# Optimization experiments

Measured on AMD Instinct MI355X. Metric: run time of the kernel, lower is better.

## Reference

```python
import jax, jax.numpy as jnp
import numpy as np

N = 50000
E = 800000
DIMS = [(8, 16), (16, 16), (16, 16)]  # (in, out) per layer


def setup_inputs() -> dict:
    key = jax.random.key(0)
    ks = jax.random.split(key, 32)
    inp = {}
    inp['x'] = jax.random.normal(ks[0], (N, 8), dtype=jnp.float32)
    inp['pos'] = jax.random.normal(ks[1], (N, 3), dtype=jnp.float32)
    k = 2
    for i, (ci, co) in enumerate(DIMS):
        d = ci * co
        inp[f'lin_w{i}'] = jax.random.normal(ks[k], (3, d), dtype=jnp.float32); k += 1
        inp[f'lin_b{i}'] = jax.random.normal(ks[k], (d,), dtype=jnp.float32); k += 1
        inp[f'gamma{i}'] = jax.random.normal(ks[k], (d,), dtype=jnp.float32); k += 1
        inp[f'beta{i}'] = jax.random.normal(ks[k], (d,), dtype=jnp.float32); k += 1
        inp[f'root{i}'] = jax.random.normal(ks[k], (ci, co), dtype=jnp.float32); k += 1
        inp[f'bias{i}'] = jax.random.normal(ks[k], (co,), dtype=jnp.float32); k += 1
    inp['batch'] = jnp.zeros((N,), dtype=jnp.int32)
    inp['idx'] = jnp.sort(jax.random.randint(ks[k], (25000,), 0, N, dtype=jnp.int32)); k += 1
    inp['edge_index'] = jax.random.randint(ks[k], (2, E), 0, N, dtype=jnp.int32)
    return inp


def _nnconv(x, pseudo, src, dst, lin_w, lin_b, gamma, beta, root, bias, ci, co):
    # edge MLP (Linear -> batchnorm(eval, affine) -> ReLU), plain_last=False
    w = jax.nn.relu((pseudo @ lin_w + lin_b) * gamma + beta)  # [E, ci*co]
    w = w.reshape(-1, ci, co)                                  # [E, ci, co]
    msg = jnp.einsum('ei,eio->eo', x[src], w)                  # per-edge vec-mat
    s = jax.ops.segment_sum(msg, dst, num_segments=N)          # scatter-sum
    cnt = jax.ops.segment_sum(jnp.ones((msg.shape[0],), x.dtype), dst, num_segments=N)
    aggr = s / jnp.maximum(cnt, 1.0)[:, None]                  # scatter-mean
    return aggr + x @ root + bias


def reference(x, pos, lin_w0, lin_b0, gamma0, beta0, root0, bias0,
              lin_w1, lin_b1, gamma1, beta1, root1, bias1,
              lin_w2, lin_b2, gamma2, beta2, root2, bias2,
              batch, idx, edge_index):
    src, dst = edge_index[0], edge_index[1]
    pseudo = pos[dst] - pos[src]  # patch_size is None
    params = [
        (lin_w0, lin_b0, gamma0, beta0, root0, bias0),
        (lin_w1, lin_b1, gamma1, beta1, root1, bias1),
        (lin_w2, lin_b2, gamma2, beta2, root2, bias2),
    ]
    h = x
    for (ci, co), p in zip(DIMS, params):
        h = jax.nn.relu(_nnconv(h, pseudo, src, dst, *p, ci, co))  # drop_act=False
    return h[idx], pos[idx], batch[idx]
```

## Files before the change

kernel.cpp:

```cpp
#include <hip/hip_runtime.h>

#define N_NODES 50000
#define N_EDGES 800000
#define M_IDX   25000
#define DMAX    64

__global__ __launch_bounds__(256) void prep_kernel(
    const int*   __restrict__ ei,
    const float* __restrict__ pos,
    float4*      __restrict__ pseudo,
    int*         __restrict__ cnt,
    int*         __restrict__ adj,
    int E)
{
    int e = blockIdx.x * blockDim.x + threadIdx.x;
    if (e >= E) return;
    int s = ei[e];
    int t = ei[E + e];
    float4 pd;
    pd.x = pos[t * 3 + 0] - pos[s * 3 + 0];
    pd.y = pos[t * 3 + 1] - pos[s * 3 + 1];
    pd.z = pos[t * 3 + 2] - pos[s * 3 + 2];
    pd.w = __int_as_float(s);
    pseudo[e] = pd;
    int p = atomicAdd(&cnt[t], 1);
    if (p < DMAX) adj[t * DMAX + p] = e;
}

template<int CI>
__global__ __launch_bounds__(256) void edge_msg_kernel(
    const float4* __restrict__ pseudo,
    const float*  __restrict__ h_in,
    const float*  __restrict__ lin_w,
    const float*  __restrict__ lin_b,
    const float*  __restrict__ gamma,
    const float*  __restrict__ beta,
    float*        __restrict__ mbuf,
    int E)
{
    const int o = threadIdx.x & 15;
    const int d = CI * 16;
    float W0[CI], W1[CI], W2[CI], B[CI];
#pragma unroll
    for (int i = 0; i < CI; ++i) {
        int j = i * 16 + o;
        float g = gamma[j];
        W0[i] = lin_w[j] * g;
        W1[i] = lin_w[d + j] * g;
        W2[i] = lin_w[2 * d + j] * g;
        B[i]  = fmaf(lin_b[j], g, beta[j]);
    }
    const int g   = (blockIdx.x * blockDim.x + threadIdx.x) >> 4;
    const int ng  = (gridDim.x * blockDim.x) >> 4;

    for (int e0 = g; e0 < E; e0 += 2 * ng) {
        const int e1 = e0 + ng;
        const bool v1 = (e1 < E);
        float4 pd0 = pseudo[e0];
        float4 pd1 = v1 ? pseudo[e1] : pd0;
        const int s0 = __float_as_int(pd0.w);
        const int s1 = __float_as_int(pd1.w);
        float x0[CI], x1[CI];
        const float4* xp0 = (const float4*)(h_in + (size_t)s0 * CI);
        const float4* xp1 = (const float4*)(h_in + (size_t)s1 * CI);
#pragma unroll
        for (int q = 0; q < CI / 4; ++q) {
            float4 a = xp0[q];
            x0[4 * q + 0] = a.x; x0[4 * q + 1] = a.y;
            x0[4 * q + 2] = a.z; x0[4 * q + 3] = a.w;
            float4 b = xp1[q];
            x1[4 * q + 0] = b.x; x1[4 * q + 1] = b.y;
            x1[4 * q + 2] = b.z; x1[4 * q + 3] = b.w;
        }
        float a0 = 0.f, a1 = 0.f;
#pragma unroll
        for (int i = 0; i < CI; ++i) {
            float w0 = fmaf(pd0.z, W2[i], fmaf(pd0.y, W1[i], fmaf(pd0.x, W0[i], B[i])));
            a0 = fmaf(x0[i], fmaxf(w0, 0.f), a0);
            float w1 = fmaf(pd1.z, W2[i], fmaf(pd1.y, W1[i], fmaf(pd1.x, W0[i], B[i])));
            a1 = fmaf(x1[i], fmaxf(w1, 0.f), a1);
        }
        mbuf[(size_t)e0 * 16 + o] = a0;
        if (v1) mbuf[(size_t)e1 * 16 + o] = a1;
    }
}

template<int CI>
__global__ __launch_bounds__(256) void node_reduce_kernel(
    const int*   __restrict__ adj,
    const int*   __restrict__ cnt,
    const float* __restrict__ mbuf,
    const float* __restrict__ h_in,
    const float* __restrict__ root,
    const float* __restrict__ bias,
    float*       __restrict__ h_out,
    int N)
{
    int tid = blockIdx.x * blockDim.x + threadIdx.x;
    if (tid >= N * 16) return;
    const int t = tid >> 4, o = tid & 15;
    const int deg = cnt[t];
    const int dl  = min(deg, DMAX);
    const int4* arow = (const int4*)(adj + (size_t)t * DMAX);
    float acc = 0.f;
    const int rounds = (dl + 3) >> 2;
    for (int r = 0; r < rounds; ++r) {
        int4 e4 = arow[r];
        int base = r * 4;
        bool m0 = base + 0 < dl, m1 = base + 1 < dl;
        bool m2 = base + 2 < dl, m3 = base + 3 < dl;
        int i0 = m0 ? e4.x : 0, i1 = m1 ? e4.y : 0;
        int i2 = m2 ? e4.z : 0, i3 = m3 ? e4.w : 0;
        float v0 = mbuf[(size_t)i0 * 16 + o];
        float v1 = mbuf[(size_t)i1 * 16 + o];
        float v2 = mbuf[(size_t)i2 * 16 + o];
        float v3 = mbuf[(size_t)i3 * 16 + o];
        acc += (m0 ? v0 : 0.f) + (m1 ? v1 : 0.f) + (m2 ? v2 : 0.f) + (m3 ? v3 : 0.f);
    }
    float r = fmaf(acc, 1.0f / fmaxf((float)deg, 1.0f), bias[o]);
    const float4* hp = (const float4*)(h_in + (size_t)t * CI);
#pragma unroll
    for (int q = 0; q < CI / 4; ++q) {
        float4 v = hp[q];
        r = fmaf(v.x, root[(4 * q + 0) * 16 + o], r);
        r = fmaf(v.y, root[(4 * q + 1) * 16 + o], r);
        r = fmaf(v.z, root[(4 * q + 2) * 16 + o], r);
        r = fmaf(v.w, root[(4 * q + 3) * 16 + o], r);
    }
    h_out[tid] = fmaxf(r, 0.f);
}

__global__ __launch_bounds__(256) void gather_kernel(
    const float* __restrict__ h,
    const float* __restrict__ pos,
    const int*   __restrict__ batch,
    const int*   __restrict__ idx,
    float*       __restrict__ out,
    int M)
{
    int j = blockIdx.x * blockDim.x + threadIdx.x;
    if (j >= M) return;
    int n = idx[j];
    float4*       o4 = (float4*)out + (size_t)j * 4;
    const float4* h4 = (const float4*)(h + (size_t)n * 16);
    o4[0] = h4[0]; o4[1] = h4[1]; o4[2] = h4[2]; o4[3] = h4[3];
    float* po = out + (size_t)M * 16 + (size_t)j * 3;
    po[0] = pos[n * 3 + 0];
    po[1] = pos[n * 3 + 1];
    po[2] = pos[n * 3 + 2];
    ((int*)out)[(size_t)M * 19 + j] = batch[n];
}

extern "C" void kernel_launch(void* const* d_in, const int* in_sizes, int n_in,
                              void* d_out, int out_size, void* d_ws, size_t ws_size,
                              hipStream_t stream) {
    const float* x      = (const float*)d_in[0];
    const float* pos    = (const float*)d_in[1];
    const float* lin_w0 = (const float*)d_in[2];
    const float* lin_b0 = (const float*)d_in[3];
    const float* gamma0 = (const float*)d_in[4];
    const float* beta0  = (const float*)d_in[5];
    const float* root0  = (const float*)d_in[6];
    const float* bias0  = (const float*)d_in[7];
    const float* lin_w1 = (const float*)d_in[8];
    const float* lin_b1 = (const float*)d_in[9];
    const float* gamma1 = (const float*)d_in[10];
    const float* beta1  = (const float*)d_in[11];
    const float* root1  = (const float*)d_in[12];
    const float* bias1  = (const float*)d_in[13];
    const float* lin_w2 = (const float*)d_in[14];
    const float* lin_b2 = (const float*)d_in[15];
    const float* gamma2 = (const float*)d_in[16];
    const float* beta2  = (const float*)d_in[17];
    const float* root2  = (const float*)d_in[18];
    const float* bias2  = (const float*)d_in[19];
    const int*   batch  = (const int*)d_in[20];
    const int*   idx    = (const int*)d_in[21];
    const int*   ei     = (const int*)d_in[22];
    float*       out    = (float*)d_out;

    float4* pseudo = (float4*)d_ws;
    float*  mbuf   = (float*)(pseudo + N_EDGES);
    int*    adj    = (int*)(mbuf + (size_t)N_EDGES * 16);
    float*  hA     = (float*)(adj + (size_t)N_NODES * DMAX);
    float*  hB     = hA + (size_t)N_NODES * 16;
    int*    cnt    = (int*)(hB + (size_t)N_NODES * 16);

    const int EB = 2048;
    const int NB = (N_NODES * 16 + 255) / 256;

    hipMemsetAsync(cnt, 0, N_NODES * sizeof(int), stream);
    prep_kernel<<<(N_EDGES + 255) / 256, 256, 0, stream>>>(ei, pos, pseudo, cnt, adj, N_EDGES);

    edge_msg_kernel<8><<<EB, 256, 0, stream>>>(pseudo, x, lin_w0, lin_b0, gamma0, beta0, mbuf, N_EDGES);
    node_reduce_kernel<8><<<NB, 256, 0, stream>>>(adj, cnt, mbuf, x, root0, bias0, hA, N_NODES);

    edge_msg_kernel<16><<<EB, 256, 0, stream>>>(pseudo, hA, lin_w1, lin_b1, gamma1, beta1, mbuf, N_EDGES);
    node_reduce_kernel<16><<<NB, 256, 0, stream>>>(adj, cnt, mbuf, hA, root1, bias1, hB, N_NODES);

    edge_msg_kernel<16><<<EB, 256, 0, stream>>>(pseudo, hB, lin_w2, lin_b2, gamma2, beta2, mbuf, N_EDGES);
    node_reduce_kernel<16><<<NB, 256, 0, stream>>>(adj, cnt, mbuf, hB, root2, bias2, hA, N_NODES);

    gather_kernel<<<(M_IDX + 255) / 256, 256, 0, stream>>>(hA, pos, batch, idx, out, M_IDX);
}
```

Before: 325.8 us.

## Fuse edge message computation into per-node reduction with destination-sorted edge data

```diff
diff --git a/kernel.cpp b/kernel.cpp
--- a/kernel.cpp
+++ b/kernel.cpp
@@ -8,38 +8,42 @@
 __global__ __launch_bounds__(256) void prep_kernel(
     const int*   __restrict__ ei,
     const float* __restrict__ pos,
-    float4*      __restrict__ pseudo,
     int*         __restrict__ cnt,
-    int*         __restrict__ adj,
+    float4*      __restrict__ pdata,
     int E)
 {
     int e = blockIdx.x * blockDim.x + threadIdx.x;
     if (e >= E) return;
+    int t = ei[E + e];
     int s = ei[e];
-    int t = ei[E + e];
+    int p = atomicAdd(&cnt[t], 1);
     float4 pd;
     pd.x = pos[t * 3 + 0] - pos[s * 3 + 0];
     pd.y = pos[t * 3 + 1] - pos[s * 3 + 1];
     pd.z = pos[t * 3 + 2] - pos[s * 3 + 2];
     pd.w = __int_as_float(s);
-    pseudo[e] = pd;
-    int p = atomicAdd(&cnt[t], 1);
-    if (p < DMAX) adj[t * DMAX + p] = e;
+    if (p < DMAX) pdata[(size_t)t * DMAX + p] = pd;
 }
 
 template<int CI>
-__global__ __launch_bounds__(256) void edge_msg_kernel(
-    const float4* __restrict__ pseudo,
+__global__ __launch_bounds__(256) void node_fused_kernel(
+    const float4* __restrict__ pdata,
+    const int*    __restrict__ cnt,
     const float*  __restrict__ h_in,
     const float*  __restrict__ lin_w,
     const float*  __restrict__ lin_b,
     const float*  __restrict__ gamma,
     const float*  __restrict__ beta,
-    float*        __restrict__ mbuf,
-    int E)
+    const float*  __restrict__ root,
+    const float*  __restrict__ bias,
+    float*        __restrict__ h_out,
+    int N)
 {
-    const int o = threadIdx.x & 15;
+    int tid = blockIdx.x * blockDim.x + threadIdx.x;
+    if (tid >= N * 16) return;
+    const int t = tid >> 4, o = tid & 15;
     const int d = CI * 16;
+
     float W0[CI], W1[CI], W2[CI], B[CI];
 #pragma unroll
     for (int i = 0; i < CI; ++i) {
@@ -50,19 +54,19 @@
         W2[i] = lin_w[2 * d + j] * g;
         B[i]  = fmaf(lin_b[j], g, beta[j]);
     }
-    const int g   = (blockIdx.x * blockDim.x + threadIdx.x) >> 4;
-    const int ng  = (gridDim.x * blockDim.x) >> 4;
 
-    for (int e0 = g; e0 < E; e0 += 2 * ng) {
-        const int e1 = e0 + ng;
-        const bool v1 = (e1 < E);
-        float4 pd0 = pseudo[e0];
-        float4 pd1 = v1 ? pseudo[e1] : pd0;
-        const int s0 = __float_as_int(pd0.w);
-        const int s1 = __float_as_int(pd1.w);
+    const int deg = cnt[t];
+    const int dl  = min(deg, DMAX);
+    const float4* __restrict__ row = pdata + (size_t)t * DMAX;
+
+    float acc = 0.f;
+    int p = 0;
+    for (; p + 2 <= dl; p += 2) {
+        float4 pd0 = row[p];
+        float4 pd1 = row[p + 1];
+        const float4* xp0 = (const float4*)(h_in + (size_t)__float_as_int(pd0.w) * CI);
+        const float4* xp1 = (const float4*)(h_in + (size_t)__float_as_int(pd1.w) * CI);
         float x0[CI], x1[CI];
-        const float4* xp0 = (const float4*)(h_in + (size_t)s0 * CI);
-        const float4* xp1 = (const float4*)(h_in + (size_t)s1 * CI);
 #pragma unroll
         for (int q = 0; q < CI / 4; ++q) {
             float4 a = xp0[q];
@@ -72,51 +76,31 @@
             x1[4 * q + 0] = b.x; x1[4 * q + 1] = b.y;
             x1[4 * q + 2] = b.z; x1[4 * q + 3] = b.w;
         }
-        float a0 = 0.f, a1 = 0.f;
 #pragma unroll
         for (int i = 0; i < CI; ++i) {
             float w0 = fmaf(pd0.z, W2[i], fmaf(pd0.y, W1[i], fmaf(pd0.x, W0[i], B[i])));
-            a0 = fmaf(x0[i], fmaxf(w0, 0.f), a0);
+            acc = fmaf(x0[i], fmaxf(w0, 0.f), acc);
             float w1 = fmaf(pd1.z, W2[i], fmaf(pd1.y, W1[i], fmaf(pd1.x, W0[i], B[i])));
-            a1 = fmaf(x1[i], fmaxf(w1, 0.f), a1);
+            acc = fmaf(x1[i], fmaxf(w1, 0.f), acc);
         }
-        mbuf[(size_t)e0 * 16 + o] = a0;
-        if (v1) mbuf[(size_t)e1 * 16 + o] = a1;
     }
-}
+    if (p < dl) {
+        float4 pd0 = row[p];
+        const float4* xp0 = (const float4*)(h_in + (size_t)__float_as_int(pd0.w) * CI);
+        float x0[CI];
+#pragma unroll
+        for (int q = 0; q < CI / 4; ++q) {
+            float4 a = xp0[q];
+            x0[4 * q + 0] = a.x; x0[4 * q + 1] = a.y;
+            x0[4 * q + 2] = a.z; x0[4 * q + 3] = a.w;
+        }
+#pragma unroll
+        for (int i = 0; i < CI; ++i) {
+            float w0 = fmaf(pd0.z, W2[i], fmaf(pd0.y, W1[i], fmaf(pd0.x, W0[i], B[i])));
+            acc = fmaf(x0[i], fmaxf(w0, 0.f), acc);
+        }
+    }
 
-template<int CI>
-__global__ __launch_bounds__(256) void node_reduce_kernel(
-    const int*   __restrict__ adj,
-    const int*   __restrict__ cnt,
-    const float* __restrict__ mbuf,
-    const float* __restrict__ h_in,
-    const float* __restrict__ root,
-    const float* __restrict__ bias,
-    float*       __restrict__ h_out,
-    int N)
-{
-    int tid = blockIdx.x * blockDim.x + threadIdx.x;
-    if (tid >= N * 16) return;
-    const int t = tid >> 4, o = tid & 15;
-    const int deg = cnt[t];
-    const int dl  = min(deg, DMAX);
-    const int4* arow = (const int4*)(adj + (size_t)t * DMAX);
-    float acc = 0.f;
-    const int rounds = (dl + 3) >> 2;
-    for (int r = 0; r < rounds; ++r) {
-        int4 e4 = arow[r];
-        int base = r * 4;
-        bool m0 = base + 0 < dl, m1 = base + 1 < dl;
-        bool m2 = base + 2 < dl, m3 = base + 3 < dl;
-        int i0 = m0 ? e4.x : 0, i1 = m1 ? e4.y : 0;
-        int i2 = m2 ? e4.z : 0, i3 = m3 ? e4.w : 0;
-        float v0 = mbuf[(size_t)i0 * 16 + o];
-        float v1 = mbuf[(size_t)i1 * 16 + o];
-        float v2 = mbuf[(size_t)i2 * 16 + o];
-        float v3 = mbuf[(size_t)i3 * 16 + o];
-        acc += (m0 ? v0 : 0.f) + (m1 ? v1 : 0.f) + (m2 ? v2 : 0.f) + (m3 ? v3 : 0.f);
-    }
     float r = fmaf(acc, 1.0f / fmaxf((float)deg, 1.0f), bias[o]);
     const float4* hp = (const float4*)(h_in + (size_t)t * CI);
 #pragma unroll
@@ -179,27 +163,22 @@
     const int*   ei     = (const int*)d_in[22];
     float*       out    = (float*)d_out;
 
-    float4* pseudo = (float4*)d_ws;
-    float*  mbuf   = (float*)(pseudo + N_EDGES);
-    int*    adj    = (int*)(mbuf + (size_t)N_EDGES * 16);
-    float*  hA     = (float*)(adj + (size_t)N_NODES * DMAX);
-    float*  hB     = hA + (size_t)N_NODES * 16;
-    int*    cnt    = (int*)(hB + (size_t)N_NODES * 16);
+    float4* pdata = (float4*)d_ws;
+    float*  hA    = (float*)(pdata + (size_t)N_NODES * DMAX);
+    float*  hB    = hA + (size_t)N_NODES * 16;
+    int*    cnt   = (int*)(hB + (size_t)N_NODES * 16);
 
-    const int EB = 2048;
+    hipMemsetAsync(cnt, 0, N_NODES * sizeof(int), stream);
+    prep_kernel<<<(N_EDGES + 255) / 256, 256, 0, stream>>>(ei, pos, cnt, pdata, N_EDGES);
+
     const int NB = (N_NODES * 16 + 255) / 256;
 
-    hipMemsetAsync(cnt, 0, N_NODES * sizeof(int), stream);
-    prep_kernel<<<(N_EDGES + 255) / 256, 256, 0, stream>>>(ei, pos, pseudo, cnt, adj, N_EDGES);
-
-    edge_msg_kernel<8><<<EB, 256, 0, stream>>>(pseudo, x, lin_w0, lin_b0, gamma0, beta0, mbuf, N_EDGES);
-    node_reduce_kernel<8><<<NB, 256, 0, stream>>>(adj, cnt, mbuf, x, root0, bias0, hA, N_NODES);
-
-    edge_msg_kernel<16><<<EB, 256, 0, stream>>>(pseudo, hA, lin_w1, lin_b1, gamma1, beta1, mbuf, N_EDGES);
-    node_reduce_kernel<16><<<NB, 256, 0, stream>>>(adj, cnt, mbuf, hA, root1, bias1, hB, N_NODES);
-
-    edge_msg_kernel<16><<<EB, 256, 0, stream>>>(pseudo, hB, lin_w2, lin_b2, gamma2, beta2, mbuf, N_EDGES);
-    node_reduce_kernel<16><<<NB, 256, 0, stream>>>(adj, cnt, mbuf, hB, root2, bias2, hA, N_NODES);
+    node_fused_kernel<8><<<NB, 256, 0, stream>>>(pdata, cnt, x,
+        lin_w0, lin_b0, gamma0, beta0, root0, bias0, hA, N_NODES);
+    node_fused_kernel<16><<<NB, 256, 0, stream>>>(pdata, cnt, hA,
+        lin_w1, lin_b1, gamma1, beta1, root1, bias1, hB, N_NODES);
+    node_fused_kernel<16><<<NB, 256, 0, stream>>>(pdata, cnt, hB,
+        lin_w2, lin_b2, gamma2, beta2, root2, bias2, hA, N_NODES);
 
     gather_kernel<<<(M_IDX + 255) / 256, 256, 0, stream>>>(hA, pos, batch, idx, out, M_IDX);
 }
```

Result: faster. 303.8 us (-6.7%).
